# Kernel optimization log

Measured on AMD Instinct MI355X. Metric: run time of the kernel, lower is better.

Reference implementation:

```python
import jax, jax.numpy as jnp
import numpy as np

B, C, O, H, W = 8, 64, 64, 128, 128


def conv3x3(x, w, b):
    # x: [B,Cin,H,W], w: [Cout,Cin,3,3], stride 1, padding 1
    y = jax.lax.conv_general_dilated(
        x, w, window_strides=(1, 1), padding=((1, 1), (1, 1)),
        dimension_numbers=("NCHW", "OIHW", "NCHW"))
    return y + b[None, :, None, None]


def setup_inputs() -> dict:
    key = jax.random.key(0)
    ks = jax.random.split(key, 6)
    fan = C * 9
    x = jax.random.normal(ks[0], (B, C, H, W), dtype=jnp.float32)
    w_main = jax.random.normal(ks[1], (O, C, 3, 3), dtype=jnp.float32) / np.sqrt(fan)
    # small offset weights keep sampled locations near the regular grid (realistic post-training regime)
    w_offset = jax.random.normal(ks[2], (18, C, 3, 3), dtype=jnp.float32) * 0.05 / np.sqrt(fan)
    b_offset = jnp.zeros((18,), dtype=jnp.float32)
    w_mask = jax.random.normal(ks[3], (9, C, 3, 3), dtype=jnp.float32) / np.sqrt(fan)
    b_mask = jnp.zeros((9,), dtype=jnp.float32)
    return {"x": x, "w_main": w_main, "w_offset": w_offset,
            "b_offset": b_offset, "w_mask": w_mask, "b_mask": b_mask}


def deform_conv2d(x, w_main, offset, mask):
    # torchvision.ops.deform_conv2d: kernel 3x3, stride 1, pad 1, dilation 1, no bias
    Bb, Cc, Hh, Ww = x.shape
    Oo = w_main.shape[0]
    off = offset.reshape(Bb, 9, 2, Hh, Ww)
    dy, dx = off[:, :, 0], off[:, :, 1]            # [B,9,H,W]; pairs ordered (y,x), k row-major
    k = jnp.arange(9)
    kh = (k // 3 - 1).astype(x.dtype)              # kernel row offset in {-1,0,1}
    kw = (k % 3 - 1).astype(x.dtype)
    iy = jnp.arange(Hh, dtype=x.dtype)
    ix = jnp.arange(Ww, dtype=x.dtype)
    # sampling positions p = p0 + p_k + delta_p
    py = dy + iy[None, None, :, None] + kh[None, :, None, None]
    px = dx + ix[None, None, None, :] + kw[None, :, None, None]

    y0 = jnp.floor(py)
    x0 = jnp.floor(px)
    ly = py - y0
    lx = px - x0
    y0i = y0.astype(jnp.int32)
    x0i = x0.astype(jnp.int32)
    y1i = y0i + 1
    x1i = x0i + 1

    bidx = jnp.arange(Bb)[:, None, None, None]

    def corner(yi, xi, wgt):
        # zero-padding semantics: out-of-bounds neighbors contribute 0
        valid = (yi >= 0) & (yi < Hh) & (xi >= 0) & (xi < Ww)
        v = x[bidx, :, jnp.clip(yi, 0, Hh - 1), jnp.clip(xi, 0, Ww - 1)]  # [B,9,H,W,C]
        return v * (wgt * valid)[..., None]

    samp = (corner(y0i, x0i, (1 - ly) * (1 - lx))
            + corner(y0i, x1i, (1 - ly) * lx)
            + corner(y1i, x0i, ly * (1 - lx))
            + corner(y1i, x1i, ly * lx))
    samp = samp * mask[..., None]                  # modulation mask (dcn v2)
    # contract sampled patches with weights: [B,9,H,W,C] x [O,C,9] -> [B,O,H,W]
    return jnp.einsum("bkhwc,ock->bohw", samp, w_main.reshape(Oo, Cc, 9))


def reference(x, w_main, w_offset, b_offset, w_mask, b_mask):
    offset = conv3x3(x, w_offset, b_offset)                 # [B,18,H,W]
    mask = jax.nn.sigmoid(conv3x3(x, w_mask, b_mask))       # [B,9,H,W]
    return deform_conv2d(x, w_main, offset, mask)
```

## Files before the change

### kernel.cpp

```cpp
#include <hip/hip_runtime.h>
#include <math.h>

#define BB 8
#define CC 64
#define OO 64
#define HH 128
#define WW 128
#define HW (HH*WW)
#define NPIX (BB*HW)

typedef __bf16 bf16x8 __attribute__((ext_vector_type(8)));
typedef float floatx4 __attribute__((ext_vector_type(4)));
typedef float f32x2  __attribute__((ext_vector_type(2)));
typedef unsigned short ushort_t;

#define XT_BYTES  16777216
#define WT_BYTES  73728

__device__ __forceinline__ unsigned short f2b(float f) {
    unsigned u = __float_as_uint(f);
    u += 0x7fffu + ((u >> 16) & 1u);
    return (unsigned short)(u >> 16);
}

__global__ __launch_bounds__(256) void transpose_kernel(
    const float* __restrict__ x, ushort_t* __restrict__ xt)
{
    __shared__ float tile[64*129];
    int bh = blockIdx.x;
    int b = bh >> 7, h = bh & 127;
    int t = threadIdx.x;

    const float* xrow = x + ((size_t)b*CC*HH + h)*WW;
    #pragma unroll
    for (int it = 0; it < 8; ++it) {
        int c = it*8 + (t >> 5);
        int w = (t & 31) * 4;
        float4 v = *(const float4*)(xrow + (size_t)c*HW + w);
        float* dst = tile + c*129 + w;
        dst[0] = v.x; dst[1] = v.y; dst[2] = v.z; dst[3] = v.w;
    }
    __syncthreads();
    ushort_t* orow = xt + (((size_t)(b*HH + h))*WW) * CC;
    #pragma unroll
    for (int it = 0; it < 4; ++it) {
        int w  = it*32 + (t >> 3);
        int cg = t & 7;
        unsigned uu[4];
        #pragma unroll
        for (int j = 0; j < 4; ++j) {
            float lo = tile[(cg*8 + 2*j)*129 + w];
            float hi = tile[(cg*8 + 2*j + 1)*129 + w];
            uu[j] = (unsigned)f2b(lo) | ((unsigned)f2b(hi) << 16);
        }
        *(uint4*)(orow + (size_t)w*CC + cg*8) = make_uint4(uu[0],uu[1],uu[2],uu[3]);
    }
}

__global__ __launch_bounds__(256) void repack_kernel(
    const float* __restrict__ wm, const float* __restrict__ woff,
    const float* __restrict__ wmask, ushort_t* __restrict__ wt,
    ushort_t* __restrict__ wb)
{
    int i = blockIdx.x * 256 + threadIdx.x;
    if (i < 36864) {
        int o = i / 576, k = i % 576, tap = k >> 6, c = k & 63;
        wt[i] = f2b(wm[o*576 + c*9 + tap]);
    }
    int j = i - 36864;
    if (j >= 0 && j < 18432) {
        int o = j / 576, k = j % 576, tap = k >> 6, c = k & 63;
        float v = 0.f;
        if (o < 18)      v = woff[o*576 + c*9 + tap];
        else if (o < 27) v = wmask[(o-18)*576 + c*9 + tap];
        wb[j] = f2b(v);
    }
}

#define WR 12
#define WSTRIDE 72
#define OMS 29

__global__ __launch_bounds__(256) void fused_kernel(
    const ushort_t* __restrict__ xt, const ushort_t* __restrict__ wb,
    const float* __restrict__ boff, const float* __restrict__ bmsk,
    const ushort_t* __restrict__ wt, float* __restrict__ out)
{
    __shared__ ushort_t win[WR*WR*WSTRIDE];
    __shared__ ushort_t samp[64*72];
    __shared__ float    om_lds[64*OMS];

    int t = threadIdx.x;
    int lane = t & 63, wv = t >> 6;
    int bid = blockIdx.x;
    int b  = bid >> 8;
    int th = (bid >> 4) & 15;
    int tw = bid & 15;
    int h0 = th * 8, w0 = tw * 8;
    const ushort_t* xbase = xt + ((size_t)b << 20);

    for (int idx = t; idx < WR*WR*8; idx += 256) {
        int r   = idx / (WR*8);
        int rem = idx - r*(WR*8);
        int col = rem >> 3;
        int ch  = (rem & 7) << 3;
        int y = h0 + r - 2, x = w0 + col - 2;
        uint4 val = make_uint4(0,0,0,0);
        if ((unsigned)y < (unsigned)HH && (unsigned)x < (unsigned)WW)
            val = *(const uint4*)(xbase + (((y << 7) + x) << 6) + ch);
        *(uint4*)(win + (r*WR + col)*WSTRIDE + ch) = val;
    }
    __syncthreads();

    int n = lane & 15, quad = lane >> 4;

    {
        const ushort_t* wb0 = wb + n*576;
        const ushort_t* wb1 = wb + (16 + n)*576;
        floatx4 acc0 = {0.f,0.f,0.f,0.f}, acc1 = {0.f,0.f,0.f,0.f};
        int trow = wv*2 + (n >> 3);
        int tcol = n & 7;

        #pragma unroll
        for (int s = 0; s < 18; ++s) {
            int tap  = s >> 1;
            int tr   = tap / 3, tc = tap % 3;
            int coff = (s & 1)*32 + quad*8;
            int kk = tap*64 + coff;
            bf16x8 b0 = *(const bf16x8*)(wb0 + kk);
            bf16x8 b1 = *(const bf16x8*)(wb1 + kk);
            bf16x8 a = *(const bf16x8*)(win +
                ((trow + tr + 1)*WR + (tcol + tc + 1))*WSTRIDE + coff);
            acc0 = __builtin_amdgcn_mfma_f32_16x16x32_bf16(a, b0, acc0, 0, 0, 0);
            acc1 = __builtin_amdgcn_mfma_f32_16x16x32_bf16(a, b1, acc1, 0, 0, 0);
        }

        #pragma unroll
        for (int r = 0; r < 4; ++r) {
            int p = wv*16 + quad*4 + r;
            float* dst = om_lds + p*OMS;
            dst[n] = acc0[r] + boff[n];
            int o1 = 16 + n;
            if (o1 < 18) {
                dst[o1] = acc1[r] + boff[o1];
            } else if (o1 < 27) {
                float z = acc1[r] + bmsk[o1 - 18];
                dst[o1] = 1.f / (1.f + expf(-z));
            }
        }
    }
    __syncthreads();

    int pa = t >> 2, cg = t & 3;
    int ph = pa >> 3, pw = pa & 7;
    int h_a = h0 + ph, w_a = w0 + pw;
    const float* omp = om_lds + pa*OMS;

    floatx4 acc[4];
    #pragma unroll
    for (int i = 0; i < 4; ++i) acc[i] = (floatx4){0.f,0.f,0.f,0.f};
    const ushort_t* wrow = wt + (wv*16 + n)*576;

    auto computeA = [&](int k, f32x2* v2) {
        int kr = k / 3, kc = k - kr*3;
        float dy = omp[2*k], dx = omp[2*k + 1], m = omp[18 + k];
        float py = (float)(h_a + kr - 1) + dy;
        float px = (float)(w_a + kc - 1) + dx;
        float y0f = floorf(py), x0f = floorf(px);
        float ly = py - y0f, lx = px - x0f;
        int y0 = (int)y0f, x0 = (int)x0f, y1 = y0 + 1, x1 = x0 + 1;
        float vy0 = ((unsigned)y0 < (unsigned)HH) ? 1.f : 0.f;
        float vy1 = ((unsigned)y1 < (unsigned)HH) ? 1.f : 0.f;
        float vx0 = ((unsigned)x0 < (unsigned)WW) ? 1.f : 0.f;
        float vx1 = ((unsigned)x1 < (unsigned)WW) ? 1.f : 0.f;

        float cw[4] = { (1.f-ly)*(1.f-lx)*vy0*vx0*m,
                        (1.f-ly)*lx      *vy0*vx1*m,
                        ly*(1.f-lx)      *vy1*vx0*m,
                        ly*lx            *vy1*vx1*m };
        int ys[4] = { y0, y0, y1, y1 };
        int xs[4] = { x0, x1, x0, x1 };

        #pragma unroll
        for (int i = 0; i < 8; ++i) v2[i] = (f32x2){0.f, 0.f};

        #pragma unroll
        for (int cn = 0; cn < 4; ++cn) {
            int yc = min(max(ys[cn], 0), HH-1);
            int xc = min(max(xs[cn], 0), WW-1);
            int wy = yc - h0 + 2, wx = xc - w0 + 2;
            uint4 q0, q1;
            if ((unsigned)wy < (unsigned)WR && (unsigned)wx < (unsigned)WR) {
                const uint4* cp = (const uint4*)(win + (wy*WR + wx)*WSTRIDE + cg*16);
                q0 = cp[0]; q1 = cp[1];
            } else {
                const uint4* cp = (const uint4*)(xbase + (((yc << 7) + xc) << 6) + cg*16);
                q0 = cp[0]; q1 = cp[1];
            }
            unsigned d[8] = { q0.x, q0.y, q0.z, q0.w, q1.x, q1.y, q1.z, q1.w };
            float wg = cw[cn];
            #pragma unroll
            for (int j = 0; j < 8; ++j) {
                f32x2 e;
                e.x = __uint_as_float(d[j] << 16);
                e.y = __uint_as_float(d[j] & 0xffff0000u);
                v2[j] += e * wg;
            }
        }
    };

    f32x2 v2[8];
    computeA(0, v2);

    for (int k = 0; k < 9; ++k) {
        {
            unsigned uu[8];
            #pragma unroll
            for (int j = 0; j < 8; ++j)
                uu[j] = (unsigned)f2b(v2[j].x) | ((unsigned)f2b(v2[j].y) << 16);
            uint4* dst = (uint4*)(samp + pa*72 + cg*16);
            dst[0] = make_uint4(uu[0], uu[1], uu[2], uu[3]);
            dst[1] = make_uint4(uu[4], uu[5], uu[6], uu[7]);
        }
        __syncthreads();

        #pragma unroll
        for (int half = 0; half < 2; ++half) {
            bf16x8 bfrag = *(const bf16x8*)(wrow + k*64 + half*32 + quad*8);
            #pragma unroll
            for (int mt = 0; mt < 4; ++mt) {
                bf16x8 afrag = *(const bf16x8*)(samp + (mt*16 + n)*72 + half*32 + quad*8);
                acc[mt] = __builtin_amdgcn_mfma_f32_16x16x32_bf16(afrag, bfrag, acc[mt], 0, 0, 0);
            }
        }
        if (k < 8) computeA(k + 1, v2);

        __syncthreads();
    }

    float* op = out + ((size_t)b*OO + (wv*16 + n))*HW;
    #pragma unroll
    for (int mt = 0; mt < 4; ++mt) {
        int row = h0 + mt*2 + (quad >> 1);
        int col = w0 + (quad & 1)*4;
        float4 st = make_float4(acc[mt][0], acc[mt][1], acc[mt][2], acc[mt][3]);
        *(float4*)(op + row*WW + col) = st;
    }
}

extern "C" void kernel_launch(void* const* d_in, const int* in_sizes, int n_in,
                              void* d_out, int out_size, void* d_ws, size_t ws_size,
                              hipStream_t stream)
{
    const float* x      = (const float*)d_in[0];
    const float* w_main = (const float*)d_in[1];
    const float* w_off  = (const float*)d_in[2];
    const float* b_off  = (const float*)d_in[3];
    const float* w_msk  = (const float*)d_in[4];
    const float* b_msk  = (const float*)d_in[5];
    float* out = (float*)d_out;

    unsigned char* ws = (unsigned char*)d_ws;
    ushort_t* xt = (ushort_t*)ws;
    ushort_t* wt = (ushort_t*)(ws + XT_BYTES);
    ushort_t* wb = (ushort_t*)(ws + XT_BYTES + WT_BYTES);

    transpose_kernel<<<BB*HH, 256, 0, stream>>>(x, xt);

    repack_kernel<<<(36864 + 18432 + 255)/256, 256, 0, stream>>>(
        w_main, w_off, w_msk, wt, wb);

    fused_kernel<<<NPIX/64, 256, 0, stream>>>(xt, wb, b_off, b_msk, wt, out);
}
```

Before: 171.2 us.

## Remove transpose pass; load NCHW fp32 input directly into bf16 LDS window

Drops the separate transpose kernel that wrote a channels-last bf16 copy of x to the workspace. The fused kernel now reads the original NCHW fp32 input directly, converting it to bf16 while filling the 12x12 shared-memory halo window. Out-of-window bilinear samples fall back to strided fp32 global loads across channels. This removes a full-tensor write and read plus a launch, but the window fill and the fallback gathers now use strided, poorly coalesced per-channel loads instead of 16-byte vector loads.

```diff
diff --git a/kernel.cpp b/kernel.cpp
--- a/kernel.cpp
+++ b/kernel.cpp
@@ -14,47 +14,12 @@
 typedef float f32x2  __attribute__((ext_vector_type(2)));
 typedef unsigned short ushort_t;
 
-#define XT_BYTES  16777216
 #define WT_BYTES  73728
 
 __device__ __forceinline__ unsigned short f2b(float f) {
     unsigned u = __float_as_uint(f);
     u += 0x7fffu + ((u >> 16) & 1u);
     return (unsigned short)(u >> 16);
-}
-
-__global__ __launch_bounds__(256) void transpose_kernel(
-    const float* __restrict__ x, ushort_t* __restrict__ xt)
-{
-    __shared__ float tile[64*129];
-    int bh = blockIdx.x;
-    int b = bh >> 7, h = bh & 127;
-    int t = threadIdx.x;
-
-    const float* xrow = x + ((size_t)b*CC*HH + h)*WW;
-    #pragma unroll
-    for (int it = 0; it < 8; ++it) {
-        int c = it*8 + (t >> 5);
-        int w = (t & 31) * 4;
-        float4 v = *(const float4*)(xrow + (size_t)c*HW + w);
-        float* dst = tile + c*129 + w;
-        dst[0] = v.x; dst[1] = v.y; dst[2] = v.z; dst[3] = v.w;
-    }
-    __syncthreads();
-    ushort_t* orow = xt + (((size_t)(b*HH + h))*WW) * CC;
-    #pragma unroll
-    for (int it = 0; it < 4; ++it) {
-        int w  = it*32 + (t >> 3);
-        int cg = t & 7;
-        unsigned uu[4];
-        #pragma unroll
-        for (int j = 0; j < 4; ++j) {
-            float lo = tile[(cg*8 + 2*j)*129 + w];
-            float hi = tile[(cg*8 + 2*j + 1)*129 + w];
-            uu[j] = (unsigned)f2b(lo) | ((unsigned)f2b(hi) << 16);
-        }
-        *(uint4*)(orow + (size_t)w*CC + cg*8) = make_uint4(uu[0],uu[1],uu[2],uu[3]);
-    }
 }
 
 __global__ __launch_bounds__(256) void repack_kernel(
@@ -82,7 +47,7 @@
 #define OMS 29
 
 __global__ __launch_bounds__(256) void fused_kernel(
-    const ushort_t* __restrict__ xt, const ushort_t* __restrict__ wb,
+    const float* __restrict__ x, const ushort_t* __restrict__ wb,
     const float* __restrict__ boff, const float* __restrict__ bmsk,
     const ushort_t* __restrict__ wt, float* __restrict__ out)
 {
@@ -97,18 +62,34 @@
     int th = (bid >> 4) & 15;
     int tw = bid & 15;
     int h0 = th * 8, w0 = tw * 8;
-    const ushort_t* xbase = xt + ((size_t)b << 20);
-
-    for (int idx = t; idx < WR*WR*8; idx += 256) {
-        int r   = idx / (WR*8);
-        int rem = idx - r*(WR*8);
-        int col = rem >> 3;
-        int ch  = (rem & 7) << 3;
-        int y = h0 + r - 2, x = w0 + col - 2;
-        uint4 val = make_uint4(0,0,0,0);
-        if ((unsigned)y < (unsigned)HH && (unsigned)x < (unsigned)WW)
-            val = *(const uint4*)(xbase + (((y << 7) + x) << 6) + ch);
-        *(uint4*)(win + (r*WR + col)*WSTRIDE + ch) = val;
+    const float* xb = x + ((size_t)b*CC << 14);
+
+    {
+        int half = t >> 7;
+        int p    = t & 127;
+        #pragma unroll
+        for (int rep = 0; rep < 2; ++rep) {
+            int pos = rep ? (128 + p) : p;
+            if (rep && p >= 16) break;
+            int r = pos / WR, col = pos - r*WR;
+            int y = h0 + r - 2, xw = w0 + col - 2;
+            bool valid = ((unsigned)y < (unsigned)HH) &&
+                         ((unsigned)xw < (unsigned)WW);
+            const float* xp = xb + ((size_t)(half*32) << 14) + (y << 7) + xw;
+            ushort_t* wp = win + pos*WSTRIDE + half*32;
+            #pragma unroll
+            for (int g = 0; g < 4; ++g) {
+                unsigned uu[4];
+                #pragma unroll
+                for (int q = 0; q < 4; ++q) {
+                    int c = g*8 + 2*q;
+                    float lo = valid ? xp[(size_t)c << 14]       : 0.f;
+                    float hi = valid ? xp[(size_t)(c+1) << 14]   : 0.f;
+                    uu[q] = (unsigned)f2b(lo) | ((unsigned)f2b(hi) << 16);
+                }
+                *(uint4*)(wp + g*8) = make_uint4(uu[0], uu[1], uu[2], uu[3]);
+            }
+        }
     }
     __syncthreads();
 
@@ -189,22 +170,27 @@
             int yc = min(max(ys[cn], 0), HH-1);
             int xc = min(max(xs[cn], 0), WW-1);
             int wy = yc - h0 + 2, wx = xc - w0 + 2;
-            uint4 q0, q1;
+            float wg = cw[cn];
             if ((unsigned)wy < (unsigned)WR && (unsigned)wx < (unsigned)WR) {
                 const uint4* cp = (const uint4*)(win + (wy*WR + wx)*WSTRIDE + cg*16);
-                q0 = cp[0]; q1 = cp[1];
+                uint4 q0 = cp[0], q1 = cp[1];
+                unsigned d[8] = { q0.x, q0.y, q0.z, q0.w, q1.x, q1.y, q1.z, q1.w };
+                #pragma unroll
+                for (int j = 0; j < 8; ++j) {
+                    f32x2 e;
+                    e.x = __uint_as_float(d[j] << 16);
+                    e.y = __uint_as_float(d[j] & 0xffff0000u);
+                    v2[j] += e * wg;
+                }
             } else {
-                const uint4* cp = (const uint4*)(xbase + (((yc << 7) + xc) << 6) + cg*16);
-                q0 = cp[0]; q1 = cp[1];
-            }
-            unsigned d[8] = { q0.x, q0.y, q0.z, q0.w, q1.x, q1.y, q1.z, q1.w };
-            float wg = cw[cn];
-            #pragma unroll
-            for (int j = 0; j < 8; ++j) {
-                f32x2 e;
-                e.x = __uint_as_float(d[j] << 16);
-                e.y = __uint_as_float(d[j] & 0xffff0000u);
-                v2[j] += e * wg;
+                const float* cp = xb + ((size_t)(cg*16) << 14) + (yc << 7) + xc;
+                #pragma unroll
+                for (int j = 0; j < 8; ++j) {
+                    f32x2 e;
+                    e.x = cp[(size_t)(2*j)   << 14];
+                    e.y = cp[(size_t)(2*j+1) << 14];
+                    v2[j] += e * wg;
+                }
             }
         }
     };
@@ -261,14 +247,11 @@
     float* out = (float*)d_out;
 
     unsigned char* ws = (unsigned char*)d_ws;
-    ushort_t* xt = (ushort_t*)ws;
-    ushort_t* wt = (ushort_t*)(ws + XT_BYTES);
-    ushort_t* wb = (ushort_t*)(ws + XT_BYTES + WT_BYTES);
-
-    transpose_kernel<<<BB*HH, 256, 0, stream>>>(x, xt);
+    ushort_t* wt = (ushort_t*)ws;
+    ushort_t* wb = (ushort_t*)(ws + WT_BYTES);
 
     repack_kernel<<<(36864 + 18432 + 255)/256, 256, 0, stream>>>(
         w_main, w_off, w_msk, wt, wb);
 
-    fused_kernel<<<NPIX/64, 256, 0, stream>>>(xt, wb, b_off, b_msk, wt, out);
-}
+    fused_kernel<<<NPIX/64, 256, 0, stream>>>(x, wb, b_off, b_msk, wt, out);
+}
```

Result: slower. 181.1 us (+5.7%).
